# Kernel tuning notes

Measured on AMD Instinct MI355X. Metric: run time of the kernel, lower is better.

The kernel has to match this reference:

```python
import jax, jax.numpy as jnp
import numpy as np

N_NODES = 50000
N_EDGES = 800000
IN_F = 128
HID = 32
HEADS = 8
CLASSES = 2
NEG_SLOPE = 0.2


def gat_conv(x, W, att_src, att_dst, bias, src, dst, heads, out_ch):
    """PyG GATConv (concat=True, add_self_loops already in src/dst).
    x: [N, F_in], W: [F_in, heads*out_ch], att_*: [heads, out_ch], bias: [heads*out_ch].
    """
    N = x.shape[0]
    h = (x @ W).reshape(N, heads, out_ch)                 # [N, H, C]
    a_src = jnp.einsum('nhc,hc->nh', h, att_src)          # [N, H]
    a_dst = jnp.einsum('nhc,hc->nh', h, att_dst)          # [N, H]
    alpha = jax.nn.leaky_relu(a_src[src] + a_dst[dst], NEG_SLOPE)  # [Etot, H]
    # segment softmax over incoming edges of each destination node
    m = jax.ops.segment_max(alpha, dst, num_segments=N)   # [N, H]
    m = jnp.where(jnp.isfinite(m), m, 0.0)
    e = jnp.exp(alpha - m[dst])                           # [Etot, H]
    s = jax.ops.segment_sum(e, dst, num_segments=N)       # [N, H]
    w = e / s[dst]                                        # [Etot, H] (self-loops guarantee s>0)
    out = jax.ops.segment_sum(h[src] * w[:, :, None], dst, num_segments=N)  # [N, H, C]
    return out.reshape(N, heads * out_ch) + bias


def setup_inputs() -> dict:
    key = jax.random.key(0)
    ks = jax.random.split(key, 12)
    x = jax.random.normal(ks[0], (N_NODES, IN_F), dtype=jnp.float32)
    edge_index = jax.random.randint(ks[1], (2, N_EDGES), 0, N_NODES, dtype=jnp.int64)
    g1 = float(np.sqrt(2.0 / (IN_F + HEADS * HID)))
    g2 = float(np.sqrt(2.0 / (HEADS * HID + CLASSES)))
    W1 = jax.random.normal(ks[2], (IN_F, HEADS * HID), dtype=jnp.float32) * g1
    att_src1 = jax.random.normal(ks[3], (HEADS, HID), dtype=jnp.float32) * 0.1
    att_dst1 = jax.random.normal(ks[4], (HEADS, HID), dtype=jnp.float32) * 0.1
    b1 = jnp.zeros((HEADS * HID,), dtype=jnp.float32)
    W2 = jax.random.normal(ks[5], (HEADS * HID, 1 * CLASSES), dtype=jnp.float32) * g2
    att_src2 = jax.random.normal(ks[6], (1, CLASSES), dtype=jnp.float32) * 0.1
    att_dst2 = jax.random.normal(ks[7], (1, CLASSES), dtype=jnp.float32) * 0.1
    b2 = jnp.zeros((CLASSES,), dtype=jnp.float32)
    return {"x": x, "edge_index": edge_index, "W1": W1, "att_src1": att_src1,
            "att_dst1": att_dst1, "b1": b1, "W2": W2, "att_src2": att_src2,
            "att_dst2": att_dst2, "b2": b2}


def reference(x, edge_index, W1, att_src1, att_dst1, b1, W2, att_src2, att_dst2, b2):
    N = x.shape[0]
    loop = jnp.arange(N, dtype=edge_index.dtype)
    src = jnp.concatenate([edge_index[0], loop])  # add self-loops (PyG default)
    dst = jnp.concatenate([edge_index[1], loop])
    h = jax.nn.relu(gat_conv(x, W1, att_src1, att_dst1, b1, src, dst, HEADS, HID))
    # dropout p=0 in eval -> identity
    out = gat_conv(h, W2, att_src2, att_dst2, b2, src, dst, 1, CLASSES)
    return out
```

## Files before the change

### kernel.cpp

```cpp
#include <hip/hip_runtime.h>
#include <hip/hip_fp16.h>

#define F_IN 128
#define C1 256
#define NEG 0.2f
#define LOG2E 1.4426950408889634f
#define SCAP 32

typedef _Float16 f16x8 __attribute__((ext_vector_type(8)));
typedef _Float16 f16x4 __attribute__((ext_vector_type(4)));
typedef float f32x4 __attribute__((ext_vector_type(4)));

#define XS_LD 136

__global__ __launch_bounds__(256) void prep_k(const float* __restrict__ W,
                                              const float* __restrict__ as1,
                                              const float* __restrict__ ad1,
                                              _Float16* __restrict__ FragW,
                                              _Float16* __restrict__ FragAtt,
                                              int* __restrict__ deg2, int N2) {
    int idx = blockIdx.x * 256 + threadIdx.x;
    if (idx < 4096) {
        int lane = idx & 63;
        int ct = (idx >> 6) & 15;
        int ks = idx >> 10;
        int kb = ks * 32 + (lane >> 4) * 8;
        int col = ct * 16 + (lane & 15);
        f16x8 v;
#pragma unroll
        for (int e = 0; e < 8; ++e)
            v[e] = (_Float16)W[(size_t)(kb + e) * C1 + col];
        *(f16x8*)(FragW + (size_t)idx * 8) = v;
    }
    if (idx < 512) {
        int lane = idx & 63;
        int ks = idx >> 6;
        int kb = ks * 32 + (lane >> 4) * 8;
        int j = lane & 15;
        f16x8 v;
#pragma unroll
        for (int e = 0; e < 8; ++e) {
            int k = kb + e;
            int hd = k >> 5;
            float val = (j < 8) ? (hd == j ? as1[k] : 0.f)
                                : (hd == (j - 8) ? ad1[k] : 0.f);
            v[e] = (_Float16)(val * LOG2E);
        }
        *(f16x8*)(FragAtt + (size_t)idx * 8) = v;
    }
    for (int i = idx; i < N2; i += gridDim.x * 256) deg2[i] = 0;
}

__global__ __launch_bounds__(256) void gemm_att_k(
        const float* __restrict__ x, const _Float16* __restrict__ FragW,
        const _Float16* __restrict__ FragAtt,
        __half* __restrict__ hh, float* __restrict__ asrc, float* __restrict__ adst,
        int N) {
    __shared__ _Float16 xs[64 * XS_LD];
    const int t = threadIdx.x;
    const int row0 = blockIdx.x * 64;
    {
        const int r = t >> 2;
        const int c0 = (t & 3) * 32;
        const int gr = row0 + r;
        _Float16* dst = xs + r * XS_LD + c0;
        if (gr < N) {
            const float4* px = (const float4*)(x + (size_t)gr * F_IN + c0);
#pragma unroll
            for (int i = 0; i < 8; ++i) {
                float4 v = px[i];
                f16x4 w;
                w[0] = (_Float16)v.x; w[1] = (_Float16)v.y;
                w[2] = (_Float16)v.z; w[3] = (_Float16)v.w;
                *(f16x4*)(dst + i * 4) = w;
            }
        } else {
            f16x4 z = {0, 0, 0, 0};
#pragma unroll
            for (int i = 0; i < 8; ++i) *(f16x4*)(dst + i * 4) = z;
        }
    }
    __syncthreads();

    const int wid = t >> 6;
    const int lane = t & 63;
    const int l15 = lane & 15;
    const int grp = lane >> 4;
    f32x4 acc[16];
#pragma unroll
    for (int i = 0; i < 16; ++i) acc[i] = (f32x4){0.f, 0.f, 0.f, 0.f};

    const _Float16* arow_p = xs + (wid * 16 + l15) * XS_LD;
    const _Float16* fwl = FragW + (size_t)lane * 8;
#pragma unroll
    for (int ks = 0; ks < 4; ++ks) {
        f16x8 afr = *(const f16x8*)(arow_p + ks * 32 + grp * 8);
#pragma unroll
        for (int ct = 0; ct < 16; ++ct) {
            f16x8 bfr = *(const f16x8*)(fwl + (((ks * 16 + ct) << 9)));
            acc[ct] = __builtin_amdgcn_mfma_f32_16x16x32_f16(afr, bfr, acc[ct], 0, 0, 0);
        }
    }
    __syncthreads();

    f32x4 acca = (f32x4){0.f, 0.f, 0.f, 0.f};
#pragma unroll
    for (int H = 0; H < 2; ++H) {
        {
            _Float16* base = xs + (wid * 16 + grp * 4) * XS_LD + l15;
#pragma unroll
            for (int c8 = 0; c8 < 8; ++c8) {
                int ct = H * 8 + c8;
#pragma unroll
                for (int i = 0; i < 4; ++i)
                    base[i * XS_LD + c8 * 16] = (_Float16)acc[ct][i];
            }
        }
        __syncthreads();
#pragma unroll
        for (int q = 0; q < 4; ++q) {
            int c = q * 256 + t;
            int rl = c >> 4;
            int cc = c & 15;
            int gr = row0 + rl;
            if (gr < N) {
                f16x8 v = *(const f16x8*)(xs + rl * XS_LD + cc * 8);
                *(f16x8*)(hh + (size_t)gr * C1 + H * 128 + cc * 8) = v;
            }
        }
        const _Float16* hrow_p = xs + (wid * 16 + l15) * XS_LD;
#pragma unroll
        for (int ksl = 0; ksl < 4; ++ksl) {
            f16x8 af = *(const f16x8*)(hrow_p + ksl * 32 + grp * 8);
            f16x8 bf = *(const f16x8*)(FragAtt + (size_t)(((H * 4 + ksl) << 6) + lane) * 8);
            acca = __builtin_amdgcn_mfma_f32_16x16x32_f16(af, bf, acca, 0, 0, 0);
        }
        __syncthreads();
    }
#pragma unroll
    for (int i = 0; i < 4; ++i) {
        int gr = row0 + wid * 16 + grp * 4 + i;
        if (gr < N) {
            if (l15 < 8) asrc[gr * 8 + l15] = acca[i];
            else         adst[gr * 8 + (l15 - 8)] = acca[i];
        }
    }
}

__global__ __launch_bounds__(256) void scat_k(const int* __restrict__ ei,
                                              int* __restrict__ deg2,
                                              unsigned short* __restrict__ ssrc,
                                              int E, int N, int nch) {
    const int part = blockIdx.x & 7;
    const int chunk = blockIdx.x >> 3;
    const float pscale = 8.0f / (float)N;
    const int CH = (E + nch - 1) / nch;
    const int b = chunk * CH;
    const int e = min(b + CH, E);
    for (int i = b + threadIdx.x; i < e; i += 256) {
        int d = ei[E + i];
        int p = (int)((float)d * pscale);
        if (p != part) continue;
        int s = ei[i];
        int sh = i & 1;
        int slot = atomicAdd(&deg2[d * 2 + sh], 1);
        slot = min(slot, SCAP - 1);
        ssrc[(d << 6) + sh * SCAP + slot] = (unsigned short)s;
    }
}

__global__ __launch_bounds__(256) void agg1_k(const __half* __restrict__ hh,
                                              const float* __restrict__ asrc,
                                              const float* __restrict__ adst,
                                              const int* __restrict__ deg2,
                                              const unsigned short* __restrict__ ssrc,
                                              const float* __restrict__ b1,
                                              const float* __restrict__ W2,
                                              const float* __restrict__ as2,
                                              const float* __restrict__ ad2,
                                              float4* __restrict__ tab2, int N) {
    const int lane = threadIdx.x & 63;
    const int n = blockIdx.x * 4 + (threadIdx.x >> 6);
    if (n >= N) return;
    const int half = lane >> 5;
    const int l5 = lane & 31;
    const int hd = l5 >> 2;
    const int ch0 = l5 * 8;
    const int xoff = l5 * 16;
    const int hoff = hd * 4;
    const char* hb = (const char*)hh;
    const char* ab = (const char*)asrc;
    const float adn = adst[n * 8 + hd];

    float ssum = 0.f;
    float4 acc0 = make_float4(0.f, 0.f, 0.f, 0.f);
    float4 acc1 = make_float4(0.f, 0.f, 0.f, 0.f);

#define PAIR(sv) do {                                                         \
    int sA_ = half ? ((int)((sv) >> 16)) : ((int)((sv) & 0xffffu));           \
    f16x8 g_ = *(const f16x8*)(hb + (sA_ << 9) + xoff);                       \
    float a_ = *(const float*)(ab + (sA_ << 5) + hoff) + adn;                 \
    float w_ = exp2f(fmaxf(a_, NEG * a_));                                    \
    ssum += w_;                                                               \
    acc0.x += (float)g_[0] * w_; acc0.y += (float)g_[1] * w_;                 \
    acc0.z += (float)g_[2] * w_; acc0.w += (float)g_[3] * w_;                 \
    acc1.x += (float)g_[4] * w_; acc1.y += (float)g_[5] * w_;                 \
    acc1.z += (float)g_[6] * w_; acc1.w += (float)g_[7] * w_; } while (0)

#define SINGLE(s0) do {                                                       \
    int sA_ = (s0);                                                           \
    f16x8 g_ = *(const f16x8*)(hb + (sA_ << 9) + xoff);                       \
    float a_ = *(const float*)(ab + (sA_ << 5) + hoff) + adn;                 \
    float w_ = exp2f(fmaxf(a_, NEG * a_));                                    \
    if (half) w_ = 0.f;                                                       \
    ssum += w_;                                                               \
    acc0.x += (float)g_[0] * w_; acc0.y += (float)g_[1] * w_;                 \
    acc0.z += (float)g_[2] * w_; acc0.w += (float)g_[3] * w_;                 \
    acc1.x += (float)g_[4] * w_; acc1.y += (float)g_[5] * w_;                 \
    acc1.z += (float)g_[6] * w_; acc1.w += (float)g_[7] * w_; } while (0)

    SINGLE(n);

#pragma unroll
    for (int seg = 0; seg < 2; ++seg) {
        const int dg = min(deg2[n * 2 + seg], SCAP);
        const unsigned short* sp = ssrc + (n << 6) + seg * SCAP;
        int j = 0;
        for (; j + 3 < dg; j += 4) {
            uint2 sv = *(const uint2*)((const unsigned int*)sp + (j >> 1));
            PAIR(sv.x);
            PAIR(sv.y);
        }
        if (j + 1 < dg) {
            unsigned int sv = *((const unsigned int*)sp + (j >> 1));
            PAIR(sv);
            j += 2;
        }
        if (j < dg) SINGLE((int)sp[j]);
    }
#undef PAIR
#undef SINGLE

    acc0.x += __shfl_xor(acc0.x, 32); acc0.y += __shfl_xor(acc0.y, 32);
    acc0.z += __shfl_xor(acc0.z, 32); acc0.w += __shfl_xor(acc0.w, 32);
    acc1.x += __shfl_xor(acc1.x, 32); acc1.y += __shfl_xor(acc1.y, 32);
    acc1.z += __shfl_xor(acc1.z, 32); acc1.w += __shfl_xor(acc1.w, 32);
    ssum += __shfl_xor(ssum, 32);

    const float inv = 1.f / ssum;
    float4 bva = *(const float4*)(b1 + ch0);
    float4 bvb = *(const float4*)(b1 + ch0 + 4);
    float o0 = fmaxf(acc0.x * inv + bva.x, 0.f);
    float o1 = fmaxf(acc0.y * inv + bva.y, 0.f);
    float o2 = fmaxf(acc0.z * inv + bva.z, 0.f);
    float o3 = fmaxf(acc0.w * inv + bva.w, 0.f);
    float o4 = fmaxf(acc1.x * inv + bvb.x, 0.f);
    float o5 = fmaxf(acc1.y * inv + bvb.y, 0.f);
    float o6 = fmaxf(acc1.z * inv + bvb.z, 0.f);
    float o7 = fmaxf(acc1.w * inv + bvb.w, 0.f);

    const float4* w2p = (const float4*)(W2 + ch0 * 2);
    float4 q0 = w2p[0], q1 = w2p[1], q2 = w2p[2], q3 = w2p[3];
    float p0 = o0 * q0.x + o1 * q0.z + o2 * q1.x + o3 * q1.z
             + o4 * q2.x + o5 * q2.z + o6 * q3.x + o7 * q3.z;
    float p1 = o0 * q0.y + o1 * q0.w + o2 * q1.y + o3 * q1.w
             + o4 * q2.y + o5 * q2.w + o6 * q3.y + o7 * q3.w;
    if (half) { p0 = 0.f; p1 = 0.f; }
#pragma unroll
    for (int off = 1; off < 64; off <<= 1) {
        p0 += __shfl_xor(p0, off);
        p1 += __shfl_xor(p1, off);
    }
    if (lane == 0) {
        float a2s = (p0 * as2[0] + p1 * as2[1]) * LOG2E;
        float a2d = (p0 * ad2[0] + p1 * ad2[1]) * LOG2E;
        tab2[n] = make_float4(p0, p1, a2s, a2d);
    }
}

__global__ __launch_bounds__(256) void agg2_k(const int* __restrict__ deg2,
                                              const unsigned short* __restrict__ ssrc,
                                              const float4* __restrict__ tab2,
                                              const float* __restrict__ b2,
                                              float* __restrict__ out, int N) {
    const int t = threadIdx.x;
    const int sub = t & 7;
    const int n = blockIdx.x * 32 + (t >> 3);
    if (n >= N) return;
    const float4 tn = tab2[n];
    const float a2d = tn.w;
    float ssum = 0.f, a0 = 0.f, a1 = 0.f;
    if (sub == 0) {
        float a = tn.z + a2d;
        a = fmaxf(a, NEG * a);
        float ev = exp2f(a);
        ssum = ev; a0 = tn.x * ev; a1 = tn.y * ev;
    }
#pragma unroll
    for (int seg = 0; seg < 2; ++seg) {
        const int dg = min(deg2[n * 2 + seg], SCAP);
        const unsigned short* sp = ssrc + (n << 6) + seg * SCAP;
        for (int j = sub; j < dg; j += 8) {
            float4 tv = tab2[sp[j]];
            float a = tv.z + a2d;
            a = fmaxf(a, NEG * a);
            float ev = exp2f(a);
            ssum += ev;
            a0 += tv.x * ev;
            a1 += tv.y * ev;
        }
    }
#pragma unroll
    for (int off = 1; off < 8; off <<= 1) {
        ssum += __shfl_xor(ssum, off);
        a0 += __shfl_xor(a0, off);
        a1 += __shfl_xor(a1, off);
    }
    if (sub == 0) {
        float inv = 1.f / ssum;
        out[(size_t)n * 2 + 0] = a0 * inv + b2[0];
        out[(size_t)n * 2 + 1] = a1 * inv + b2[1];
    }
}

extern "C" void kernel_launch(void* const* d_in, const int* in_sizes, int n_in,
                              void* d_out, int out_size, void* d_ws, size_t ws_size,
                              hipStream_t stream) {
    const float* x   = (const float*)d_in[0];
    const int*   ei  = (const int*)d_in[1];
    const float* W1  = (const float*)d_in[2];
    const float* at_s1 = (const float*)d_in[3];
    const float* at_d1 = (const float*)d_in[4];
    const float* b1  = (const float*)d_in[5];
    const float* W2  = (const float*)d_in[6];
    const float* at_s2 = (const float*)d_in[7];
    const float* at_d2 = (const float*)d_in[8];
    const float* b2  = (const float*)d_in[9];
    float* out = (float*)d_out;

    const int N = in_sizes[0] / F_IN;
    const int E = in_sizes[1] / 2;

    char* ws = (char*)d_ws;
    size_t off = 0;
    auto alloc = [&](size_t bytes) -> void* {
        void* p = ws + off;
        off = (off + bytes + 255) & ~(size_t)255;
        return p;
    };
    __half*          hh      = (__half*)alloc((size_t)N * C1 * 2);
    _Float16*        FragW   = (_Float16*)alloc((size_t)4096 * 8 * 2);
    _Float16*        FragAtt = (_Float16*)alloc((size_t)512 * 8 * 2);
    float*           asrc    = (float*)alloc((size_t)N * 8 * 4);
    float*           adst    = (float*)alloc((size_t)N * 8 * 4);
    int*             deg2    = (int*)alloc((size_t)N * 2 * 4);
    unsigned short*  ssrc    = (unsigned short*)alloc((size_t)N * 64 * 2);
    float4*          tab2    = (float4*)alloc((size_t)N * 16);

    prep_k<<<64, 256, 0, stream>>>(W1, at_s1, at_d1, FragW, FragAtt,
                                   deg2, N * 2);
    const int nbg = (N + 63) / 64;
    gemm_att_k<<<nbg, 256, 0, stream>>>(x, FragW, FragAtt, hh, asrc, adst, N);
    const int nch = (E + 1023) / 1024;
    scat_k<<<nch * 8, 256, 0, stream>>>(ei, deg2, ssrc, E, N, nch);
    agg1_k<<<(N + 3) / 4, 256, 0, stream>>>(hh, asrc, adst, deg2, ssrc,
                                            b1, W2, at_s2, at_d2, tab2, N);
    agg2_k<<<(N + 31) / 32, 256, 0, stream>>>(deg2, ssrc, tab2, b2, out, N);
}
```

Baseline: 156.0 us.

## Fuse GEMM and edge-scatter kernels into one interleaved launch

Merges the node-feature GEMM/attention kernel and the edge scatter kernel into a single launch. Block indices are interleaved so that out of every 9 groups of 8 blocks, 8 groups do scatter work and 1 group does GEMM tiles. The two independent phases can then run concurrently on the GPU and one launch boundary goes away. The cost is some idle blocks that exit early, and shared-memory allocation for scatter blocks that do not use it, which may limit occupancy.

Result: no change. 157.2 us (+0.8%).

```diff
diff --git a/kernel.cpp b/kernel.cpp
--- a/kernel.cpp
+++ b/kernel.cpp
@@ -51,21 +51,52 @@
     for (int i = idx; i < N2; i += gridDim.x * 256) deg2[i] = 0;
 }
 
-__global__ __launch_bounds__(256) void gemm_att_k(
+__global__ __launch_bounds__(256) void gemm_scat_k(
         const float* __restrict__ x, const _Float16* __restrict__ FragW,
         const _Float16* __restrict__ FragAtt,
         __half* __restrict__ hh, float* __restrict__ asrc, float* __restrict__ adst,
-        int N) {
+        const int* __restrict__ ei, int* __restrict__ deg2,
+        unsigned short* __restrict__ ssrc,
+        int N, int E, int nbg, int nch) {
+    const int b = blockIdx.x;
+    const int group = b >> 3;
+    const int sub = b & 7;
+    const int gq = group / 9;
+    const int gr = group % 9;
     __shared__ _Float16 xs[64 * XS_LD];
+
+    if (gr != 8) {
+        const int chunk = group - gq;
+        if (chunk >= nch) return;
+        const int part = sub;
+        const float pscale = 8.0f / (float)N;
+        const int CH = (E + nch - 1) / nch;
+        const int beg = chunk * CH;
+        const int end = min(beg + CH, E);
+        for (int i = beg + threadIdx.x; i < end; i += 256) {
+            int d = ei[E + i];
+            int p = (int)((float)d * pscale);
+            if (p != part) continue;
+            int s = ei[i];
+            int sh = i & 1;
+            int slot = atomicAdd(&deg2[d * 2 + sh], 1);
+            slot = min(slot, SCAP - 1);
+            ssrc[(d << 6) + sh * SCAP + slot] = (unsigned short)s;
+        }
+        return;
+    }
+
+    const int g = gq * 8 + sub;
+    if (g >= nbg) return;
     const int t = threadIdx.x;
-    const int row0 = blockIdx.x * 64;
+    const int row0 = g * 64;
     {
         const int r = t >> 2;
         const int c0 = (t & 3) * 32;
-        const int gr = row0 + r;
+        const int grow = row0 + r;
         _Float16* dst = xs + r * XS_LD + c0;
-        if (gr < N) {
-            const float4* px = (const float4*)(x + (size_t)gr * F_IN + c0);
+        if (grow < N) {
+            const float4* px = (const float4*)(x + (size_t)grow * F_IN + c0);
 #pragma unroll
             for (int i = 0; i < 8; ++i) {
                 float4 v = px[i];
@@ -122,10 +153,10 @@
             int c = q * 256 + t;
             int rl = c >> 4;
             int cc = c & 15;
-            int gr = row0 + rl;
-            if (gr < N) {
+            int grow = row0 + rl;
+            if (grow < N) {
                 f16x8 v = *(const f16x8*)(xs + rl * XS_LD + cc * 8);
-                *(f16x8*)(hh + (size_t)gr * C1 + H * 128 + cc * 8) = v;
+                *(f16x8*)(hh + (size_t)grow * C1 + H * 128 + cc * 8) = v;
             }
         }
         const _Float16* hrow_p = xs + (wid * 16 + l15) * XS_LD;
@@ -139,33 +170,11 @@
     }
 #pragma unroll
     for (int i = 0; i < 4; ++i) {
-        int gr = row0 + wid * 16 + grp * 4 + i;
-        if (gr < N) {
-            if (l15 < 8) asrc[gr * 8 + l15] = acca[i];
-            else         adst[gr * 8 + (l15 - 8)] = acca[i];
-        }
-    }
-}
-
-__global__ __launch_bounds__(256) void scat_k(const int* __restrict__ ei,
-                                              int* __restrict__ deg2,
-                                              unsigned short* __restrict__ ssrc,
-                                              int E, int N, int nch) {
-    const int part = blockIdx.x & 7;
-    const int chunk = blockIdx.x >> 3;
-    const float pscale = 8.0f / (float)N;
-    const int CH = (E + nch - 1) / nch;
-    const int b = chunk * CH;
-    const int e = min(b + CH, E);
-    for (int i = b + threadIdx.x; i < e; i += 256) {
-        int d = ei[E + i];
-        int p = (int)((float)d * pscale);
-        if (p != part) continue;
-        int s = ei[i];
-        int sh = i & 1;
-        int slot = atomicAdd(&deg2[d * 2 + sh], 1);
-        slot = min(slot, SCAP - 1);
-        ssrc[(d << 6) + sh * SCAP + slot] = (unsigned short)s;
+        int grow = row0 + wid * 16 + grp * 4 + i;
+        if (grow < N) {
+            if (l15 < 8) asrc[grow * 8 + l15] = acca[i];
+            else         adst[grow * 8 + (l15 - 8)] = acca[i];
+        }
     }
 }
 
@@ -359,10 +368,14 @@
 
     prep_k<<<64, 256, 0, stream>>>(W1, at_s1, at_d1, FragW, FragAtt,
                                    deg2, N * 2);
+
     const int nbg = (N + 63) / 64;
-    gemm_att_k<<<nbg, 256, 0, stream>>>(x, FragW, FragAtt, hh, asrc, adst, N);
     const int nch = (E + 1023) / 1024;
-    scat_k<<<nch * 8, 256, 0, stream>>>(ei, deg2, ssrc, E, N, nch);
+    const int ngg = (nbg + 7) / 8;
+    const int M = (ngg > (nch + 7) / 8) ? ngg : (nch + 7) / 8;
+    const int G = M * 9;
+    gemm_scat_k<<<G * 8, 256, 0, stream>>>(x, FragW, FragAtt, hh, asrc, adst,
+                                           ei, deg2, ssrc, N, E, nbg, nch);
     agg1_k<<<(N + 3) / 4, 256, 0, stream>>>(hh, asrc, adst, deg2, ssrc,
                                             b1, W2, at_s2, at_d2, tab2, N);
     agg2_k<<<(N + 31) / 32, 256, 0, stream>>>(deg2, ssrc, tab2, b2, out, N);
```
